# Kernel optimization log

Measured on AMD Instinct MI355X. Metric: run time of the kernel, lower is better.

Reference implementation:

```python
import jax, jax.numpy as jnp
import numpy as np

B, S, H, DH = 8, 2048, 16, 64
D = H * DH  # 1024; also the input feature dim
BIG_NEG = 1e8


def setup_inputs() -> dict:
    key = jax.random.key(0)
    ks = jax.random.split(key, 7)
    glorot = lambda k, shp: jax.random.normal(k, shp, jnp.float32) * np.sqrt(2.0 / (shp[0] + shp[1]))
    return {
        "Q_seq": jax.random.normal(ks[0], (B, S, D), jnp.float32),
        "K_seq": jax.random.normal(ks[1], (B, S, D), jnp.float32),
        "Q_mask": jnp.ones((B, S), jnp.float32),
        "K_mask": jnp.ones((B, S), jnp.float32),
        "WQ": glorot(ks[2], (D, D)),
        "WK": glorot(ks[3], (D, D)),
        "Wq": glorot(ks[4], (D, H)),
        "Wk": glorot(ks[5], (D, H)),
        "WP": glorot(ks[6], (D, D)),
    }


def reference(Q_seq, B_K_seq=None, **_unused):
    raise NotImplementedError  # placeholder overwritten below


def reference(Q_seq, K_seq, Q_mask, K_mask, WQ, WK, Wq, Wk, WP):
    scale = 1.0 / (DH ** 0.5)
    b, s, _ = Q_seq.shape

    Q = Q_seq @ WQ                                        # (B,S,D)
    # query additive attention over the sequence, per head
    q_logits = jnp.einsum('bsd,dh->bhs', Q, Wq) * scale   # (B,H,S)
    q_logits = q_logits - (1.0 - Q_mask[:, None, :]) * BIG_NEG
    q_att = jax.nn.softmax(q_logits, axis=-1)

    Qh = Q.reshape(b, s, H, DH).transpose(0, 2, 1, 3)     # (B,H,S,DH)
    Kh = (K_seq @ WK).reshape(b, s, H, DH).transpose(0, 2, 1, 3)

    global_q = jnp.einsum('bhs,bhsd->bhd', q_att, Qh)     # (B,H,DH)
    QK = Kh * global_q[:, :, None, :]                     # (B,H,S,DH)

    # NOTE: original reshapes (B,H,S,DH) straight to (B,S,H*DH) WITHOUT a
    # transpose (head-mixing raw reshape) — replicated faithfully here.
    QK_flat = QK.reshape(b, s, H * DH)
    k_logits = jnp.einsum('bsd,dh->bhs', QK_flat, Wk) * scale
    k_logits = k_logits - (1.0 - K_mask[:, None, :]) * BIG_NEG
    k_att = jax.nn.softmax(k_logits, axis=-1)

    global_k = jnp.einsum('bhs,bhsd->bhd', k_att, QK)     # (B,H,DH)
    QKQ = global_k[:, :, None, :] * Qh                    # (B,H,S,DH)

    out = QKQ.transpose(0, 2, 1, 3).reshape(b, s, H * DH) @ WP
    out = out.reshape(b, s, H, DH).transpose(0, 2, 1, 3) + Qh   # (B,H,S,DH)
    out = out.transpose(0, 2, 1, 3).reshape(b, s, H * DH)       # (B,S,D)
    return out
```

## Files before the change

kernel.cpp:

```cpp
#include <hip/hip_runtime.h>
#include <cstdint>
#include <cstddef>


#define B_ 8
#define S_ 2048
#define H_ 16
#define D_ 1024
#define SCALE_ 0.125f
#define BIGNEG_ 1e8f

typedef __attribute__((ext_vector_type(8))) __bf16 bf16x8;
typedef __attribute__((ext_vector_type(4))) float f32x4;

__device__ __forceinline__ unsigned short f2bf(float f) {
  unsigned int u = __float_as_uint(f);
  u += 0x7FFFu + ((u >> 16) & 1u);
  return (unsigned short)(u >> 16);
}
__device__ __forceinline__ float bf2f(unsigned short h) {
  return __uint_as_float(((unsigned int)h) << 16);
}

__device__ __forceinline__ void gll16(const void* g, void* l) {
  __builtin_amdgcn_global_load_lds(
      (__attribute__((address_space(1))) void*)(uintptr_t)g,
      (__attribute__((address_space(3))) void*)(uintptr_t)l,
      16, 0, 0);
}

__global__ __launch_bounds__(256) void k_conv2(
    const float* __restrict__ in0, unsigned short* __restrict__ out0,
    const float* __restrict__ in1, unsigned short* __restrict__ out1, int n4) {
  int i = blockIdx.x * 256 + threadIdx.x;
  const float* in = in0;
  unsigned short* out = out0;
  if (i >= n4) { i -= n4; in = in1; out = out1; }
  float4 v = ((const float4*)in)[i];
  ushort4 o;
  o.x = f2bf(v.x); o.y = f2bf(v.y); o.z = f2bf(v.z); o.w = f2bf(v.w);
  ((ushort4*)out)[i] = o;
}

__global__ __launch_bounds__(256) void k_transpose3(
    const float* __restrict__ s0, unsigned short* __restrict__ d0,
    const float* __restrict__ s1, unsigned short* __restrict__ d1,
    const float* __restrict__ s2, unsigned short* __restrict__ d2,
    int K, int N) {
  const float* src = blockIdx.z == 0 ? s0 : (blockIdx.z == 1 ? s1 : s2);
  unsigned short* dst = blockIdx.z == 0 ? d0 : (blockIdx.z == 1 ? d1 : d2);
  __shared__ float tile[32][33];
  int n0 = blockIdx.x * 32, k0 = blockIdx.y * 32;
  int tx = threadIdx.x, ty = threadIdx.y;
#pragma unroll
  for (int i = 0; i < 4; i++) {
    int r = ty + i * 8;
    if (k0 + r < K && n0 + tx < N) tile[r][tx] = src[(size_t)(k0 + r) * N + n0 + tx];
  }
  __syncthreads();
#pragma unroll
  for (int i = 0; i < 4; i++) {
    int rn = ty + i * 8;
    if (n0 + rn < N && k0 + tx < K)
      dst[(size_t)(n0 + rn) * K + k0 + tx] = f2bf(tile[tx][rn]);
  }
}

__global__ __launch_bounds__(256) void k_transpose2(
    const float* __restrict__ s0, unsigned short* __restrict__ d0,
    const float* __restrict__ s1, unsigned short* __restrict__ d1,
    int K, int N) {
  const float* src = blockIdx.z == 0 ? s0 : s1;
  unsigned short* dst = blockIdx.z == 0 ? d0 : d1;
  __shared__ float tile[32][33];
  int n0 = blockIdx.x * 32, k0 = blockIdx.y * 32;
  int tx = threadIdx.x, ty = threadIdx.y;
#pragma unroll
  for (int i = 0; i < 4; i++) {
    int r = ty + i * 8;
    if (k0 + r < K && n0 + tx < N) tile[r][tx] = src[(size_t)(k0 + r) * N + n0 + tx];
  }
  __syncthreads();
#pragma unroll
  for (int i = 0; i < 4; i++) {
    int rn = ty + i * 8;
    if (n0 + rn < N && k0 + tx < K)
      dst[(size_t)(n0 + rn) * K + k0 + tx] = f2bf(tile[tx][rn]);
  }
}

__global__ __launch_bounds__(256) void k_gemm128(
    const unsigned short* __restrict__ A, const unsigned short* __restrict__ Aalt,
    int asplit,
    const unsigned short* __restrict__ BTa, const unsigned short* __restrict__ BTb,
    int bstride,
    unsigned short* __restrict__ Cbf, unsigned short* __restrict__ Calt,
    float* __restrict__ Cf, const unsigned short* __restrict__ Res,
    int N, int K, int ntiles) {
  __shared__ unsigned short lA[128 * 64];
  __shared__ unsigned short lB[128 * 64];
  int t = threadIdx.x;
  int mt = blockIdx.x / ntiles, nt = blockIdx.x - mt * ntiles;
  const unsigned short* BT = BTa;
  unsigned short* Cb = Cbf;
  if (mt >= asplit) { mt -= asplit; A = Aalt; BT = BTb; Cb = Calt; }
  if (bstride) BT += (size_t)(mt >> 4) * bstride;
  int m0 = mt * 128, n0 = nt * 128;
  int lane = t & 63, w = t >> 6;
  int wm = (w >> 1) * 64, wn = (w & 1) * 64;
  int mq = lane & 15, q = lane >> 4;

  f32x4 zero = {0.f, 0.f, 0.f, 0.f};
  f32x4 acc[4][4];
#pragma unroll
  for (int i = 0; i < 4; i++)
#pragma unroll
    for (int j = 0; j < 4; j++) acc[i][j] = zero;

  const unsigned short* gA[4];
  const unsigned short* gB[4];
  unsigned short* pA[4];
  unsigned short* pB[4];
#pragma unroll
  for (int p = 0; p < 4; p++) {
    int g = t + p * 256;
    int row = g >> 3, cg = (g & 7) ^ (row & 7);
    gA[p] = A + (size_t)(m0 + row) * K + cg * 8;
    gB[p] = BT + (size_t)(n0 + row) * K + cg * 8;
    pA[p] = &lA[g * 8];
    pB[p] = &lB[g * 8];
  }

  int xa = mq & 7;
  for (int k0 = 0; k0 < K; k0 += 64) {
#pragma unroll
    for (int p = 0; p < 4; p++) gll16(gA[p] + k0, pA[p]);
#pragma unroll
    for (int p = 0; p < 4; p++) gll16(gB[p] + k0, pB[p]);
    __syncthreads();
#pragma unroll
    for (int kk = 0; kk < 2; kk++) {
      int xo = ((kk * 4 + q) ^ xa) * 8;
      bf16x8 av[4], bv[4];
#pragma unroll
      for (int i = 0; i < 4; i++)
        av[i] = *(const bf16x8*)&lA[(wm + i * 16 + mq) * 64 + xo];
#pragma unroll
      for (int i = 0; i < 4; i++)
        bv[i] = *(const bf16x8*)&lB[(wn + i * 16 + mq) * 64 + xo];
#pragma unroll
      for (int i = 0; i < 4; i++)
#pragma unroll
        for (int j = 0; j < 4; j++)
          acc[i][j] = __builtin_amdgcn_mfma_f32_16x16x32_bf16(av[i], bv[j], acc[i][j], 0, 0, 0);
    }
    __syncthreads();
  }

#pragma unroll
  for (int i = 0; i < 4; i++)
#pragma unroll
    for (int j = 0; j < 4; j++)
#pragma unroll
      for (int r = 0; r < 4; r++) {
        int row = m0 + wm + i * 16 + q * 4 + r;
        int col = n0 + wn + j * 16 + mq;
        size_t o = (size_t)row * N + col;
        float v = acc[i][j][r];
        if (Res) v += bf2f(Res[o]);
        if (Cf) Cf[o] = v;
        if (Cb) Cb[o] = f2bf(v);
      }
}

__global__ __launch_bounds__(256) void k_logits16(
    const unsigned short* __restrict__ A,
    const unsigned short* __restrict__ BT16,
    const float* __restrict__ mask,
    float* __restrict__ outl,
    int K) {
  __shared__ unsigned short lA[64 * 32];
  int t = threadIdx.x;
  int m0 = blockIdx.x * 64;
  int lane = t & 63, w = t >> 6;
  int mq = lane & 15, q = lane >> 4;
  f32x4 acc = {0.f, 0.f, 0.f, 0.f};
  const unsigned short* gA = A + (size_t)(m0 + (t >> 2)) * K + (t & 3) * 8;
  unsigned short* pA = &lA[t * 8];
  for (int k0 = 0; k0 < K; k0 += 32) {
    gll16(gA + k0, pA);
    bf16x8 bv = *(const bf16x8*)&BT16[(size_t)mq * K + k0 + q * 8];
    __syncthreads();
    bf16x8 a0 = *(const bf16x8*)&lA[(w * 16 + mq) * 32 + q * 8];
    acc = __builtin_amdgcn_mfma_f32_16x16x32_bf16(a0, bv, acc, 0, 0, 0);
    __syncthreads();
  }
#pragma unroll
  for (int r = 0; r < 4; r++) {
    int row = m0 + w * 16 + q * 4 + r;
    int b = row >> 11, s = row & 2047;
    float v = acc[r] * SCALE_ - (1.0f - mask[row]) * BIGNEG_;
    outl[((size_t)(b * 16 + mq)) * 2048 + s] = v;
  }
}

__global__ __launch_bounds__(256) void k_logits16g(
    const unsigned short* __restrict__ Khbf,
    const unsigned short* __restrict__ WkT,
    const float* __restrict__ gq,
    const float* __restrict__ mask,
    float* __restrict__ outl) {
  __shared__ unsigned short lA[64 * 32];
  int t = threadIdx.x;
  int m0 = blockIdx.x * 64;
  int bb = m0 >> 11;
  int h2 = (m0 >> 7) & 15;
  int half = (m0 >> 6) & 1;
  int lane = t & 63, w = t >> 6;
  int mq = lane & 15, q = lane >> 4;
  f32x4 acc = {0.f, 0.f, 0.f, 0.f};
  int r0 = half * 64 + (t >> 2);
  int c0 = t & 3;
  const unsigned short* base = Khbf + (size_t)bb * 2048 * 1024 + h2 * 64;
  const float* gqb = gq + bb * 1024 + h2 * 64;
  unsigned short* pA = &lA[t * 8];
  for (int k0 = 0; k0 < 1024; k0 += 32) {
    int kc0 = k0 + c0 * 8;
    gll16(base + (size_t)(16 * r0 + (kc0 >> 6)) * 1024 + (kc0 & 63), pA);
    int kq = k0 + q * 8;
    bf16x8 wv = *(const bf16x8*)&WkT[(size_t)mq * 1024 + kq];
    float4 g0 = *(const float4*)&gqb[kq & 63];
    float4 g1 = *(const float4*)&gqb[(kq & 63) + 4];
    bf16x8 bv;
    bv[0] = (__bf16)((float)wv[0] * g0.x);
    bv[1] = (__bf16)((float)wv[1] * g0.y);
    bv[2] = (__bf16)((float)wv[2] * g0.z);
    bv[3] = (__bf16)((float)wv[3] * g0.w);
    bv[4] = (__bf16)((float)wv[4] * g1.x);
    bv[5] = (__bf16)((float)wv[5] * g1.y);
    bv[6] = (__bf16)((float)wv[6] * g1.z);
    bv[7] = (__bf16)((float)wv[7] * g1.w);
    __syncthreads();
    bf16x8 a0 = *(const bf16x8*)&lA[(w * 16 + mq) * 32 + q * 8];
    acc = __builtin_amdgcn_mfma_f32_16x16x32_bf16(a0, bv, acc, 0, 0, 0);
    __syncthreads();
  }
#pragma unroll
  for (int r = 0; r < 4; r++) {
    int row = m0 + w * 16 + q * 4 + r;
    int b = row >> 11, s = row & 2047;
    float v = acc[r] * SCALE_ - (1.0f - mask[row]) * BIGNEG_;
    outl[((size_t)(b * 16 + mq)) * 2048 + s] = v;
  }
}

__global__ __launch_bounds__(256) void k_softmax(float* __restrict__ logits) {
  __shared__ float red[8];
  int t = threadIdx.x;
  int lane = t & 63, w = t >> 6;
  float* lg = logits + (size_t)blockIdx.x * 2048;
  float4 a = ((const float4*)lg)[t];
  float4 b = ((const float4*)lg)[t + 256];
  float mx = fmaxf(fmaxf(fmaxf(a.x, a.y), fmaxf(a.z, a.w)),
                   fmaxf(fmaxf(b.x, b.y), fmaxf(b.z, b.w)));
#pragma unroll
  for (int off = 32; off > 0; off >>= 1) mx = fmaxf(mx, __shfl_down(mx, off, 64));
  if (lane == 0) red[w] = mx;
  __syncthreads();
  mx = fmaxf(fmaxf(red[0], red[1]), fmaxf(red[2], red[3]));
  float4 ea, eb;
  ea.x = expf(a.x - mx); ea.y = expf(a.y - mx); ea.z = expf(a.z - mx); ea.w = expf(a.w - mx);
  eb.x = expf(b.x - mx); eb.y = expf(b.y - mx); eb.z = expf(b.z - mx); eb.w = expf(b.w - mx);
  float ps = ea.x + ea.y + ea.z + ea.w + eb.x + eb.y + eb.z + eb.w;
#pragma unroll
  for (int off = 32; off > 0; off >>= 1) ps += __shfl_down(ps, off, 64);
  if (lane == 0) red[4 + w] = ps;
  __syncthreads();
  float inv = 1.0f / (red[4] + red[5] + red[6] + red[7]);
  ea.x *= inv; ea.y *= inv; ea.z *= inv; ea.w *= inv;
  eb.x *= inv; eb.y *= inv; eb.z *= inv; eb.w *= inv;
  ((float4*)lg)[t] = ea;
  ((float4*)lg)[t + 256] = eb;
}

__global__ __launch_bounds__(256) void k_poolpart(
    const float* __restrict__ att,
    const unsigned short* __restrict__ X,
    float* __restrict__ partial) {
  __shared__ float satt[32 * 16];
  int c = blockIdx.x, b = blockIdx.y;
  int t = threadIdx.x;
  for (int i = t; i < 512; i += 256) {
    int sl = i >> 4, h = i & 15;
    satt[i] = att[(((size_t)b * 16 + h) << 11) + c * 32 + sl];
  }
  __syncthreads();
  int h = t >> 4;
  const ushort4* xp = (const ushort4*)X + ((size_t)b * 2048 + c * 32) * 256 + t;
  float4 acc = {0.f, 0.f, 0.f, 0.f};
#pragma unroll 8
  for (int sl = 0; sl < 32; sl++) {
    float av = satt[sl * 16 + h];
    ushort4 xv = xp[sl * 256];
    acc.x += av * bf2f(xv.x);
    acc.y += av * bf2f(xv.y);
    acc.z += av * bf2f(xv.z);
    acc.w += av * bf2f(xv.w);
  }
  ((float4*)partial)[((size_t)b * 64 + c) * 256 + t] = acc;
}

__global__ __launch_bounds__(256) void k_poolfin(
    const float* __restrict__ partial,
    const float* __restrict__ gmul,
    float* __restrict__ outp) {
  int oi = blockIdx.x * 256 + threadIdx.x;
  int b = oi >> 10;
  const float* pp = partial + (size_t)b * 64 * 1024 + (oi & 1023);
  float s = 0.f;
#pragma unroll 8
  for (int c = 0; c < 64; c++) s += pp[(size_t)c * 1024];
  if (gmul) s *= gmul[oi];
  outp[oi] = s;
}

__global__ __launch_bounds__(256) void k_wpb(
    const unsigned short* __restrict__ WPT,
    const float* __restrict__ gk,
    unsigned short* __restrict__ WPb) {
  int i = blockIdx.x * 256 + threadIdx.x;
  int flat4 = i * 4;
  int b = flat4 >> 20;
  int rem = flat4 & 1048575;
  int k = rem & 1023;
  ushort4 wv = *(const ushort4*)&WPT[rem];
  float4 gv = *(const float4*)&gk[b * 1024 + k];
  ushort4 o;
  o.x = f2bf(bf2f(wv.x) * gv.x);
  o.y = f2bf(bf2f(wv.y) * gv.y);
  o.z = f2bf(bf2f(wv.z) * gv.z);
  o.w = f2bf(bf2f(wv.w) * gv.w);
  *(ushort4*)&WPb[flat4] = o;
}

extern "C" void kernel_launch(void* const* d_in, const int* in_sizes, int n_in,
                              void* d_out, int out_size, void* d_ws, size_t ws_size,
                              hipStream_t stream) {
  const float* Qseq  = (const float*)d_in[0];
  const float* Kseq  = (const float*)d_in[1];
  const float* Qmask = (const float*)d_in[2];
  const float* Kmask = (const float*)d_in[3];
  const float* WQ    = (const float*)d_in[4];
  const float* WK    = (const float*)d_in[5];
  const float* Wq    = (const float*)d_in[6];
  const float* Wk    = (const float*)d_in[7];
  const float* WP    = (const float*)d_in[8];
  float* out = (float*)d_out;

  const size_t SD = (size_t)B_ * S_ * D_;
  unsigned short* Qbf  = (unsigned short*)d_ws;
  unsigned short* Khbf = Qbf + SD;
  unsigned short* buf0 = Khbf + SD;
  unsigned short* WQT  = buf0 + SD;
  unsigned short* WKT  = WQT + (size_t)D_ * D_;
  unsigned short* WPT  = WKT + (size_t)D_ * D_;
  unsigned short* WqT  = WPT + (size_t)D_ * D_;
  unsigned short* WkT  = WqT + (size_t)H_ * D_;
  float* ql = (float*)(WkT + (size_t)H_ * D_);
  float* kl = ql + (size_t)B_ * H_ * S_;
  float* gq = kl + (size_t)B_ * H_ * S_;
  float* gk = gq + (size_t)B_ * D_;
  float* partial = (float*)buf0;
  unsigned short* WPb = buf0 + 2 * 1024 * 1024;
  unsigned short* Kstage = (unsigned short*)d_out;

  dim3 blk256(256);
  dim3 tblk(32, 8);
  int n4 = (int)(SD / 4);

  k_transpose3<<<dim3(32, 32, 3), tblk, 0, stream>>>(WQ, WQT, WK, WKT, WP, WPT, D_, D_);
  k_transpose2<<<dim3(1, 32, 2), tblk, 0, stream>>>(Wq, WqT, Wk, WkT, D_, H_);

  k_conv2<<<dim3(2 * ((n4 + 255) / 256)), blk256, 0, stream>>>(Qseq, buf0, Kseq, Kstage, n4);

  k_gemm128<<<dim3(2048), blk256, 0, stream>>>(buf0, Kstage, 128, WQT, WKT, 0,
                                               Qbf, Khbf, (float*)nullptr,
                                               (const unsigned short*)nullptr, D_, D_, 8);

  k_logits16<<<dim3(256), blk256, 0, stream>>>(Qbf, WqT, Qmask, ql, D_);
  k_softmax<<<dim3(128), blk256, 0, stream>>>(ql);
  k_poolpart<<<dim3(64, 8), blk256, 0, stream>>>(ql, Qbf, partial);
  k_poolfin<<<dim3(32), blk256, 0, stream>>>(partial, (const float*)nullptr, gq);

  k_logits16g<<<dim3(256), blk256, 0, stream>>>(Khbf, WkT, gq, Kmask, kl);
  k_softmax<<<dim3(128), blk256, 0, stream>>>(kl);
  k_poolpart<<<dim3(64, 8), blk256, 0, stream>>>(kl, Khbf, partial);
  k_poolfin<<<dim3(32), blk256, 0, stream>>>(partial, gq, gk);

  k_wpb<<<dim3(8192), blk256, 0, stream>>>(WPT, gk, WPb);
  k_gemm128<<<dim3(1024), blk256, 0, stream>>>(Qbf, Qbf, 1 << 30, WPb, WPb, 1 << 20,
                                               (unsigned short*)nullptr, (unsigned short*)nullptr,
                                               out, Qbf, D_, D_, 8);
}
```

Before: 434.0 us.

## Replace 128x128 GEMM with 256x256-tile double-buffered pipelined GEMM

Swaps the 128x128 GEMM (256 threads, single LDS buffer, two barriers per k-step) for a 256x256 tile kernel with 512 threads that double-buffers 32-wide k slices in LDS. Global loads for slice it+2 are issued while MFMAs run on the current slice, governed by explicit vmcnt waits, and MFMA issue priority is raised. Block indices are remapped across groups of 8 to improve L2 locality. The larger tile gives more reuse per load but leaves fewer blocks (512 and 256) to fill the CUs and raises register pressure from 32 accumulators per thread.

```diff
diff --git a/kernel.cpp b/kernel.cpp
--- a/kernel.cpp
+++ b/kernel.cpp
@@ -89,82 +89,112 @@
   }
 }
 
-__global__ __launch_bounds__(256) void k_gemm128(
+__global__ __launch_bounds__(512, 2) void k_gemm256(
     const unsigned short* __restrict__ A, const unsigned short* __restrict__ Aalt,
     int asplit,
     const unsigned short* __restrict__ BTa, const unsigned short* __restrict__ BTb,
-    int bstride,
+    int bstride, int bshift,
     unsigned short* __restrict__ Cbf, unsigned short* __restrict__ Calt,
     float* __restrict__ Cf, const unsigned short* __restrict__ Res,
     int N, int K, int ntiles) {
-  __shared__ unsigned short lA[128 * 64];
-  __shared__ unsigned short lB[128 * 64];
+  __shared__ unsigned short lds[32768];
   int t = threadIdx.x;
-  int mt = blockIdx.x / ntiles, nt = blockIdx.x - mt * ntiles;
+  int lid = (blockIdx.x & 7) * ((int)gridDim.x >> 3) + (blockIdx.x >> 3);
+  int mt = lid / ntiles, nt = lid - mt * ntiles;
   const unsigned short* BT = BTa;
   unsigned short* Cb = Cbf;
   if (mt >= asplit) { mt -= asplit; A = Aalt; BT = BTb; Cb = Calt; }
-  if (bstride) BT += (size_t)(mt >> 4) * bstride;
-  int m0 = mt * 128, n0 = nt * 128;
+  if (bstride) BT += (size_t)(mt >> bshift) * (size_t)bstride;
+  int m0 = mt * 256, n0 = nt * 256;
   int lane = t & 63, w = t >> 6;
-  int wm = (w >> 1) * 64, wn = (w & 1) * 64;
+  int wr = (w >> 2) * 128;
+  int wc = (w & 3) * 64;
   int mq = lane & 15, q = lane >> 4;
 
   f32x4 zero = {0.f, 0.f, 0.f, 0.f};
-  f32x4 acc[4][4];
-#pragma unroll
-  for (int i = 0; i < 4; i++)
+  f32x4 acc[8][4];
+#pragma unroll
+  for (int i = 0; i < 8; i++)
 #pragma unroll
     for (int j = 0; j < 4; j++) acc[i][j] = zero;
 
-  const unsigned short* gA[4];
-  const unsigned short* gB[4];
-  unsigned short* pA[4];
-  unsigned short* pB[4];
-#pragma unroll
-  for (int p = 0; p < 4; p++) {
-    int g = t + p * 256;
-    int row = g >> 3, cg = (g & 7) ^ (row & 7);
-    gA[p] = A + (size_t)(m0 + row) * K + cg * 8;
-    gB[p] = BT + (size_t)(n0 + row) * K + cg * 8;
-    pA[p] = &lA[g * 8];
-    pB[p] = &lB[g * 8];
-  }
-
-  int xa = mq & 7;
-  for (int k0 = 0; k0 < K; k0 += 64) {
-#pragma unroll
-    for (int p = 0; p < 4; p++) gll16(gA[p] + k0, pA[p]);
-#pragma unroll
-    for (int p = 0; p < 4; p++) gll16(gB[p] + k0, pB[p]);
-    __syncthreads();
-#pragma unroll
-    for (int kk = 0; kk < 2; kk++) {
-      int xo = ((kk * 4 + q) ^ xa) * 8;
-      bf16x8 av[4], bv[4];
-#pragma unroll
-      for (int i = 0; i < 4; i++)
-        av[i] = *(const bf16x8*)&lA[(wm + i * 16 + mq) * 64 + xo];
-#pragma unroll
-      for (int i = 0; i < 4; i++)
-        bv[i] = *(const bf16x8*)&lB[(wn + i * 16 + mq) * 64 + xo];
-#pragma unroll
-      for (int i = 0; i < 4; i++)
-#pragma unroll
-        for (int j = 0; j < 4; j++)
-          acc[i][j] = __builtin_amdgcn_mfma_f32_16x16x32_bf16(av[i], bv[j], acc[i][j], 0, 0, 0);
+  const unsigned short* gA[2];
+  const unsigned short* gB[2];
+  int oA[2], oB[2];
+#pragma unroll
+  for (int p = 0; p < 2; p++) {
+    int g = t + p * 512;
+    int row2 = g >> 3, pre = (g & 7) ^ (row2 & 7);
+    int r = row2 * 2 + (pre >> 2), oct = pre & 3;
+    gA[p] = A + (size_t)(m0 + r) * K + oct * 8;
+    gB[p] = BT + (size_t)(n0 + r) * K + oct * 8;
+    oA[p] = g * 8;
+    oB[p] = 8192 + g * 8;
+  }
+
+  int sA8 = ((((mq & 1) << 2) | q) ^ (mq >> 1)) * 8;
+  int ra = (wr >> 1) + (mq >> 1);
+  int rb = (wc >> 1) + (mq >> 1);
+
+  int NT = K >> 5;
+#pragma unroll
+  for (int p = 0; p < 2; p++) gll16(gA[p], &lds[oA[p]]);
+#pragma unroll
+  for (int p = 0; p < 2; p++) gll16(gB[p], &lds[oB[p]]);
+#pragma unroll
+  for (int p = 0; p < 2; p++) gll16(gA[p] + 32, &lds[16384 + oA[p]]);
+#pragma unroll
+  for (int p = 0; p < 2; p++) gll16(gB[p] + 32, &lds[16384 + oB[p]]);
+
+  for (int it = 0; it < NT; ++it) {
+    int lbase = (it & 1) << 14;
+    if (it < NT - 1) {
+      asm volatile("s_waitcnt vmcnt(4)" ::: "memory");
+    } else {
+      asm volatile("s_waitcnt vmcnt(0)" ::: "memory");
     }
-    __syncthreads();
-  }
-
-#pragma unroll
-  for (int i = 0; i < 4; i++)
+    __builtin_amdgcn_s_barrier();
+    __builtin_amdgcn_sched_barrier(0);
+
+    const unsigned short* la = &lds[lbase];
+    const unsigned short* lb = &lds[lbase + 8192];
+    bf16x8 av[8], bv[4];
+#pragma unroll
+    for (int i = 0; i < 8; i++)
+      av[i] = *(const bf16x8*)&la[(ra + i * 8) * 64 + sA8];
 #pragma unroll
     for (int j = 0; j < 4; j++)
+      bv[j] = *(const bf16x8*)&lb[(rb + j * 8) * 64 + sA8];
+    asm volatile("s_waitcnt lgkmcnt(0)" ::: "memory");
+    __builtin_amdgcn_sched_barrier(0);
+    __builtin_amdgcn_s_barrier();
+    __builtin_amdgcn_sched_barrier(0);
+
+    if (it + 2 < NT) {
+      int k0 = (it + 2) * 32;
+#pragma unroll
+      for (int p = 0; p < 2; p++) gll16(gA[p] + k0, &lds[lbase + oA[p]]);
+#pragma unroll
+      for (int p = 0; p < 2; p++) gll16(gB[p] + k0, &lds[lbase + oB[p]]);
+    }
+
+    __builtin_amdgcn_s_setprio(1);
+#pragma unroll
+    for (int i = 0; i < 8; i++)
+#pragma unroll
+      for (int j = 0; j < 4; j++)
+        acc[i][j] = __builtin_amdgcn_mfma_f32_16x16x32_bf16(av[i], bv[j], acc[i][j], 0, 0, 0);
+    __builtin_amdgcn_s_setprio(0);
+  }
+
+#pragma unroll
+  for (int i = 0; i < 8; i++)
+#pragma unroll
+    for (int j = 0; j < 4; j++)
 #pragma unroll
       for (int r = 0; r < 4; r++) {
-        int row = m0 + wm + i * 16 + q * 4 + r;
-        int col = n0 + wn + j * 16 + mq;
+        int row = m0 + wr + i * 16 + q * 4 + r;
+        int col = n0 + wc + j * 16 + mq;
         size_t o = (size_t)row * N + col;
         float v = acc[i][j][r];
         if (Res) v += bf2f(Res[o]);
@@ -375,6 +405,7 @@
   unsigned short* Kstage = (unsigned short*)d_out;
 
   dim3 blk256(256);
+  dim3 blk512(512);
   dim3 tblk(32, 8);
   int n4 = (int)(SD / 4);
 
@@ -383,9 +414,9 @@
 
   k_conv2<<<dim3(2 * ((n4 + 255) / 256)), blk256, 0, stream>>>(Qseq, buf0, Kseq, Kstage, n4);
 
-  k_gemm128<<<dim3(2048), blk256, 0, stream>>>(buf0, Kstage, 128, WQT, WKT, 0,
-                                               Qbf, Khbf, (float*)nullptr,
-                                               (const unsigned short*)nullptr, D_, D_, 8);
+  k_gemm256<<<dim3(512), blk512, 0, stream>>>(buf0, Kstage, 64, WQT, WKT, 0, 0,
+                                              Qbf, Khbf, (float*)nullptr,
+                                              (const unsigned short*)nullptr, D_, D_, 4);
 
   k_logits16<<<dim3(256), blk256, 0, stream>>>(Qbf, WqT, Qmask, ql, D_);
   k_softmax<<<dim3(128), blk256, 0, stream>>>(ql);
@@ -398,7 +429,7 @@
   k_poolfin<<<dim3(32), blk256, 0, stream>>>(partial, gq, gk);
 
   k_wpb<<<dim3(8192), blk256, 0, stream>>>(WPT, gk, WPb);
-  k_gemm128<<<dim3(1024), blk256, 0, stream>>>(Qbf, Qbf, 1 << 30, WPb, WPb, 1 << 20,
-                                               (unsigned short*)nullptr, (unsigned short*)nullptr,
-                                               out, Qbf, D_, D_, 8);
-}
+  k_gemm256<<<dim3(256), blk512, 0, stream>>>(Qbf, Qbf, 1 << 30, WPb, WPb, 1 << 20, 3,
+                                              (unsigned short*)nullptr, (unsigned short*)nullptr,
+                                              out, Qbf, D_, D_, 4);
+}
```

Result: faster. 390.1 us (-10.1%).
